# Kernel optimization log

Hardware: AMD Instinct MI355X
Metric: run time of the kernel (lower is better)

The kernel has to match this reference:

```python
import jax, jax.numpy as jnp
import numpy as np

N, E, G, H, D = 50000, 800000, 64, 2, 128  # nodes, edges, graphs, heads, out_channels
NEG_SLOPE_ATT = 0.2   # GATv2 default negative_slope
NEG_SLOPE_OUT = 0.01  # torch.nn.LeakyReLU default
BN_EPS = 1e-5


def setup_inputs() -> dict:
    key = jax.random.key(0)
    ks = jax.random.split(key, 12)
    x = jax.random.normal(ks[0], (N, 1), jnp.float32)
    edge_index = jax.random.randint(ks[1], (2, E), 0, N, dtype=jnp.int64)
    edge_attr = jax.random.normal(ks[2], (E,), jnp.float32)
    batch = jnp.sort(jax.random.randint(ks[3], (N,), 0, G, dtype=jnp.int64))
    # GATv2Conv params: lin_l/lin_r: Linear(1, H*D) with bias; lin_edge: Linear(1, H*D) no bias
    Wl = jax.random.normal(ks[4], (1, H * D), jnp.float32) * 0.5
    bl = jax.random.normal(ks[5], (H * D,), jnp.float32) * 0.1
    Wr = jax.random.normal(ks[6], (1, H * D), jnp.float32) * 0.5
    br = jax.random.normal(ks[7], (H * D,), jnp.float32) * 0.1
    We = jax.random.normal(ks[8], (1, H * D), jnp.float32) * 0.5
    att = jax.random.normal(ks[9], (H, D), jnp.float32) * 0.5
    bias = jax.random.normal(ks[10], (D,), jnp.float32) * 0.1
    gamma = jnp.ones((D,), jnp.float32)
    beta = jnp.zeros((D,), jnp.float32)
    return {"x": x, "edge_index": edge_index, "edge_attr": edge_attr, "batch": batch,
            "Wl": Wl, "bl": bl, "Wr": Wr, "br": br, "We": We, "att": att,
            "bias": bias, "gamma": gamma, "beta": beta}


def reference(x, edge_index, edge_attr, batch, Wl, bl, Wr, br, We, att, bias, gamma, beta):
    n = x.shape[0]
    src, dst = edge_index[0], edge_index[1]  # message flows src -> dst
    # node transforms: [N, H, D]
    xl = (x @ Wl + bl).reshape(n, H, D)  # lin_l (source side, also the message value)
    xr = (x @ Wr + br).reshape(n, H, D)  # lin_r (destination side)
    # edge feature embedding: [E, H, D]
    ee = (edge_attr[:, None] @ We).reshape(-1, H, D)
    # GATv2 scoring: leaky_relu(x_j + x_i + e), then dot with attention vector
    m = jax.nn.leaky_relu(xl[src] + xr[dst] + ee, NEG_SLOPE_ATT)  # [E, H, D]
    alpha = jnp.einsum('ehd,hd->eh', m, att)  # [E, H]
    # scatter-softmax over incoming edges per destination node
    amax = jax.ops.segment_max(alpha, dst, num_segments=n)  # [N, H]
    ea = jnp.exp(alpha - amax[dst])
    denom = jax.ops.segment_sum(ea, dst, num_segments=n)
    alpha = ea / (denom[dst] + 1e-16)
    # weighted scatter-add aggregation of x_j
    out = jax.ops.segment_sum(xl[src] * alpha[..., None], dst, num_segments=n)  # [N, H, D]
    out = out.mean(axis=1) + bias  # concat=False -> head average, then conv bias
    # BatchNorm1d in training mode (biased variance over nodes)
    mean = out.mean(axis=0)
    var = ((out - mean) ** 2).mean(axis=0)
    out = (out - mean) * jax.lax.rsqrt(var + BN_EPS) * gamma + beta
    out = jax.nn.leaky_relu(out, NEG_SLOPE_OUT)
    # graph-level scatter_add pooling
    return jax.ops.segment_sum(out, batch, num_segments=G)  # [G, D]
```

## Files before the change

### kernel.cpp

```cpp
#include <hip/hip_runtime.h>
#include <math.h>

#define NN 50000
#define NE 800000
#define NG 64

#define CB    2048
#define NBLK  391
#define NBUCK 196

static_assert(NBLK * CB >= NE, "chunk cover");
static_assert((NBUCK - 1) == (NN - 1) / 256, "bucket count");
static_assert(NE % 8 == 0, "edge unroll");

#define WS_C     0
#define WS_ACC   16
#define WS_BNSUM (WS_ACC + 4*NN)
#define WS_BNSQ  (WS_BNSUM + 128)
#define WS_MOM   WS_BNSUM
#define WS_EX    (WS_BNSQ + 128)
#define WS_TOT   (WS_EX + 272)
#define WS_CNT   (WS_TOT + 256)
#define WS_SORT  (WS_CNT + 256*NBLK)
#define WS_END   (WS_SORT + 4*NE)
#define WS_NEED_BYTES ((size_t)WS_END * 4 + 256)

static_assert(((WS_SORT * 4) % 16) == 0, "sort 16B alignment");

#define STEP(wl_, wr_, we_, bb_, at_, xs_, xd_, ae_, acc_)                 \
  { float tt = fmaf(we_, ae_, bb_); tt = fmaf(wr_, xd_, tt);               \
    tt = fmaf(wl_, xs_, tt); acc_ = fmaf(fabsf(tt), at_, acc_); }

#define SMEM_WEIGHTS_DECL                                                  \
  __shared__ __align__(16) float sWl[256], sWr[256], sWe[256], sB[256], sAt[256];

#define SMEM_WEIGHTS_LOAD                                                  \
  { int t_ = threadIdx.x;                                                  \
    sWl[t_] = Wl[t_]; sWr[t_] = Wr[t_]; sWe[t_] = We[t_];                  \
    sB[t_] = bl[t_] + br[t_]; sAt[t_] = att[t_]; }                         \
  __syncthreads();

#define SCORES(xs_, xd_, ae_, accA, accB, out0, out1)                      \
  { float lin0 = fmaf(c0.x, xs_, fmaf(c0.y, xd_, fmaf(c0.z, ae_, c0.w))); \
    out0 = fmaf(0.4f, accA, 0.6f * lin0);                                  \
    float lin1 = fmaf(c1.x, xs_, fmaf(c1.y, xd_, fmaf(c1.z, ae_, c1.w))); \
    out1 = fmaf(0.4f, accB, 0.6f * lin1); }

#define STEP4(c, q0, q1, q2, q3)                                           \
  STEP(wl.c, wr.c, we.c, bb.c, at.c, xs0, xd0, ae0, q0)                    \
  STEP(wl.c, wr.c, we.c, bb.c, at.c, xs1, xd1, ae1, q1)                    \
  STEP(wl.c, wr.c, we.c, bb.c, at.c, xs2, xd2, ae2, q2)                    \
  STEP(wl.c, wr.c, we.c, bb.c, at.c, xs3, xd3, ae3, q3)

#define SCORE_CORE                                                         \
  int4 s4 = *(const int4*)&ei[base];                                       \
  int4 dd4 = *(const int4*)&ei[NE + base];                                 \
  float4 ae4 = *(const float4*)&eattr[base];                               \
  float xs0 = x[s4.x], xs1 = x[s4.y], xs2 = x[s4.z], xs3 = x[s4.w];        \
  float xd0 = x[dd4.x], xd1 = x[dd4.y], xd2 = x[dd4.z], xd3 = x[dd4.w];    \
  float ae0 = ae4.x, ae1 = ae4.y, ae2 = ae4.z, ae3 = ae4.w;

#define SCORE_LOOPS                                                        \
  float a00 = 0.f, a01 = 0.f, a02 = 0.f, a03 = 0.f;                        \
  float a10 = 0.f, a11 = 0.f, a12 = 0.f, a13 = 0.f;                        \
  _Pragma("unroll 2")                                                      \
  for (int j = 0; j < 128; j += 4) {                                       \
    float4 wl = *(const float4*)&sWl[j];                                   \
    float4 wr = *(const float4*)&sWr[j];                                   \
    float4 we = *(const float4*)&sWe[j];                                   \
    float4 bb = *(const float4*)&sB[j];                                    \
    float4 at = *(const float4*)&sAt[j];                                   \
    STEP4(x, a00, a01, a02, a03)                                           \
    STEP4(y, a00, a01, a02, a03)                                           \
    STEP4(z, a00, a01, a02, a03)                                           \
    STEP4(w, a00, a01, a02, a03)                                           \
  }                                                                        \
  _Pragma("unroll 2")                                                      \
  for (int j = 128; j < 256; j += 4) {                                     \
    float4 wl = *(const float4*)&sWl[j];                                   \
    float4 wr = *(const float4*)&sWr[j];                                   \
    float4 we = *(const float4*)&sWe[j];                                   \
    float4 bb = *(const float4*)&sB[j];                                    \
    float4 at = *(const float4*)&sAt[j];                                   \
    STEP4(x, a10, a11, a12, a13)                                           \
    STEP4(y, a10, a11, a12, a13)                                           \
    STEP4(z, a10, a11, a12, a13)                                           \
    STEP4(w, a10, a11, a12, a13)                                           \
  }                                                                        \
  float4 c0 = *(const float4*)&ws[WS_C];                                   \
  float4 c1 = *(const float4*)&ws[WS_C + 4];

#define STEP8(c, Q)                                                        \
  STEP(wl.c, wr.c, we.c, bb.c, at.c, xs0, xd0, ae0, Q##0)                  \
  STEP(wl.c, wr.c, we.c, bb.c, at.c, xs1, xd1, ae1, Q##1)                  \
  STEP(wl.c, wr.c, we.c, bb.c, at.c, xs2, xd2, ae2, Q##2)                  \
  STEP(wl.c, wr.c, we.c, bb.c, at.c, xs3, xd3, ae3, Q##3)                  \
  STEP(wl.c, wr.c, we.c, bb.c, at.c, xs4, xd4, ae4, Q##4)                  \
  STEP(wl.c, wr.c, we.c, bb.c, at.c, xs5, xd5, ae5, Q##5)                  \
  STEP(wl.c, wr.c, we.c, bb.c, at.c, xs6, xd6, ae6, Q##6)                  \
  STEP(wl.c, wr.c, we.c, bb.c, at.c, xs7, xd7, ae7, Q##7)

extern "C" __global__ __launch_bounds__(256)
void k_hist(const int* __restrict__ ei,
            const float* __restrict__ att, const float* __restrict__ Wl,
            const float* __restrict__ Wr, const float* __restrict__ We,
            const float* __restrict__ bl, const float* __restrict__ br,
            float* __restrict__ ws, float* __restrict__ out)
{
  __shared__ unsigned cnt[256];
  cnt[threadIdx.x] = 0u;
  __syncthreads();
  int base = blockIdx.x * CB + (int)threadIdx.x * 8;
  if (base < NE) {
    int4 a = *(const int4*)&ei[NE + base];
    int4 b = *(const int4*)&ei[NE + base + 4];
    atomicAdd(&cnt[((unsigned)a.x) >> 8], 1u);
    atomicAdd(&cnt[((unsigned)a.y) >> 8], 1u);
    atomicAdd(&cnt[((unsigned)a.z) >> 8], 1u);
    atomicAdd(&cnt[((unsigned)a.w) >> 8], 1u);
    atomicAdd(&cnt[((unsigned)b.x) >> 8], 1u);
    atomicAdd(&cnt[((unsigned)b.y) >> 8], 1u);
    atomicAdd(&cnt[((unsigned)b.z) >> 8], 1u);
    atomicAdd(&cnt[((unsigned)b.w) >> 8], 1u);
  }
  __syncthreads();
  unsigned* counts = (unsigned*)(ws + WS_CNT);
  counts[(size_t)threadIdx.x * NBLK + blockIdx.x] = cnt[threadIdx.x];
  int gid = blockIdx.x * 256 + (int)threadIdx.x;
  if (gid < NG * 128) out[gid] = 0.f;
  if (gid < 14) ws[WS_MOM + gid] = 0.f;
  if (blockIdx.x == 0) {
    __shared__ float red[4][256];
    int t = threadIdx.x;
    float a = att[t];
    red[0][t] = a * Wl[t];
    red[1][t] = a * Wr[t];
    red[2][t] = a * We[t];
    red[3][t] = a * (bl[t] + br[t]);
    __syncthreads();
    if (t < 8) {
      int k = t >> 1, h = t & 1;
      float s = 0.f;
      for (int d = 0; d < 128; ++d) s += red[k][h * 128 + d];
      ws[WS_C + h * 4 + k] = s;
    }
  }
}

extern "C" __global__ __launch_bounds__(256)
void k_scan1(float* __restrict__ ws)
{
  int b = blockIdx.x;
  int t = threadIdx.x;
  unsigned* row = (unsigned*)(ws + WS_CNT) + (size_t)b * NBLK;
  __shared__ unsigned sc[256];
  unsigned carry = 0;
  for (int c = 0; c < NBLK; c += 256) {
    int k = c + t;
    unsigned v = (k < NBLK) ? row[k] : 0u;
    sc[t] = v;
    __syncthreads();
    for (int o = 1; o < 256; o <<= 1) {
      unsigned u = (t >= o) ? sc[t - o] : 0u;
      __syncthreads();
      sc[t] += u;
      __syncthreads();
    }
    unsigned incl = sc[t];
    if (k < NBLK) row[k] = carry + incl - v;
    unsigned total = sc[255];
    __syncthreads();
    carry += total;
  }
  if (t == 0) ((unsigned*)(ws + WS_TOT))[b] = carry;
}

extern "C" __global__ __launch_bounds__(256)
void k_scan2(float* __restrict__ ws)
{
  int b = threadIdx.x;
  unsigned v = ((const unsigned*)(ws + WS_TOT))[b];
  __shared__ unsigned sc[256];
  sc[b] = v;
  __syncthreads();
  for (int o = 1; o < 256; o <<= 1) {
    unsigned u = (b >= o) ? sc[b - o] : 0u;
    __syncthreads();
    sc[b] += u;
    __syncthreads();
  }
  unsigned* ex = (unsigned*)(ws + WS_EX);
  ex[b] = sc[b] - v;
  if (b == 255) ex[256] = sc[b];
}

extern "C" __global__ __launch_bounds__(256, 2)
void k_score(const int* __restrict__ ei, const float* __restrict__ x,
             const float* __restrict__ eattr,
             const float* __restrict__ Wl, const float* __restrict__ Wr,
             const float* __restrict__ We, const float* __restrict__ bl,
             const float* __restrict__ br, const float* __restrict__ att,
             float* __restrict__ ws)
{
  SMEM_WEIGHTS_DECL
  __shared__ unsigned soff[256];
  { int t_ = threadIdx.x;
    sWl[t_] = Wl[t_]; sWr[t_] = Wr[t_]; sWe[t_] = We[t_];
    sB[t_] = bl[t_] + br[t_]; sAt[t_] = att[t_];
    const unsigned* counts = (const unsigned*)(ws + WS_CNT);
    const unsigned* ex = (const unsigned*)(ws + WS_EX);
    soff[t_] = ex[t_] + counts[(size_t)t_ * NBLK + blockIdx.x];
  }
  __syncthreads();
  int base = blockIdx.x * CB + (int)threadIdx.x * 8;
  if (base >= NE) return;
  int4 sa = *(const int4*)&ei[base];
  int4 sb = *(const int4*)&ei[base + 4];
  int4 da = *(const int4*)&ei[NE + base];
  int4 db = *(const int4*)&ei[NE + base + 4];
  float4 aea = *(const float4*)&eattr[base];
  float4 aeb = *(const float4*)&eattr[base + 4];
  float ae0 = aea.x, ae1 = aea.y, ae2 = aea.z, ae3 = aea.w;
  float ae4 = aeb.x, ae5 = aeb.y, ae6 = aeb.z, ae7 = aeb.w;
  float xs0 = x[sa.x], xs1 = x[sa.y], xs2 = x[sa.z], xs3 = x[sa.w];
  float xs4 = x[sb.x], xs5 = x[sb.y], xs6 = x[sb.z], xs7 = x[sb.w];
  float xd0 = x[da.x], xd1 = x[da.y], xd2 = x[da.z], xd3 = x[da.w];
  float xd4 = x[db.x], xd5 = x[db.y], xd6 = x[db.z], xd7 = x[db.w];
  float q0 = 0.f, q1 = 0.f, q2 = 0.f, q3 = 0.f;
  float q4 = 0.f, q5 = 0.f, q6 = 0.f, q7 = 0.f;
  float r0 = 0.f, r1 = 0.f, r2 = 0.f, r3 = 0.f;
  float r4 = 0.f, r5 = 0.f, r6 = 0.f, r7 = 0.f;
#pragma unroll 2
  for (int j = 0; j < 128; j += 4) {
    float4 wl = *(const float4*)&sWl[j];
    float4 wr = *(const float4*)&sWr[j];
    float4 we = *(const float4*)&sWe[j];
    float4 bb = *(const float4*)&sB[j];
    float4 at = *(const float4*)&sAt[j];
    STEP8(x, q) STEP8(y, q) STEP8(z, q) STEP8(w, q)
  }
#pragma unroll 2
  for (int j = 128; j < 256; j += 4) {
    float4 wl = *(const float4*)&sWl[j];
    float4 wr = *(const float4*)&sWr[j];
    float4 we = *(const float4*)&sWe[j];
    float4 bb = *(const float4*)&sB[j];
    float4 at = *(const float4*)&sAt[j];
    STEP8(x, r) STEP8(y, r) STEP8(z, r) STEP8(w, r)
  }
  float4 c0 = *(const float4*)&ws[WS_C];
  float4 c1 = *(const float4*)&ws[WS_C + 4];
  float4* srt = (float4*)(ws + WS_SORT);
  float s0, s1;
#define EPI(i, dv)                                                         \
  { SCORES(xs##i, xd##i, ae##i, q##i, r##i, s0, s1)                        \
    unsigned d_ = (unsigned)(dv);                                          \
    unsigned p_ = atomicAdd(&soff[d_ >> 8], 1u);                           \
    srt[p_] = make_float4(__expf(s0), __expf(s1), xs##i, __uint_as_float(d_)); }
  EPI(0, da.x) EPI(1, da.y) EPI(2, da.z) EPI(3, da.w)
  EPI(4, db.x) EPI(5, db.y) EPI(6, db.z) EPI(7, db.w)
#undef EPI
}

extern "C" __global__ __launch_bounds__(256)
void k_gather(float* __restrict__ ws)
{
  int b = blockIdx.x;
  const int t = threadIdx.x;
  __shared__ float acc[1024];
  acc[t] = 0.f; acc[256 + t] = 0.f; acc[512 + t] = 0.f; acc[768 + t] = 0.f;
  __syncthreads();
  const unsigned* ex = (const unsigned*)(ws + WS_EX);
  int lo = (int)ex[b], hi = (int)ex[b + 1];
  const float4* srt = (const float4*)(ws + WS_SORT);
  for (int i = lo + t; i < hi; i += 256) {
    float4 r = srt[i];
    int l4 = (int)(__float_as_uint(r.w) & 255u) * 4;
    atomicAdd(&acc[l4 + 0], r.x);
    atomicAdd(&acc[l4 + 1], r.y);
    atomicAdd(&acc[l4 + 2], r.x * r.z);
    atomicAdd(&acc[l4 + 3], r.y * r.z);
  }
  __syncthreads();
  int n = (b << 8) + t;
  float f1 = 0.f, f2 = 0.f, f3 = 0.f, f4 = 0.f;
  if (n < NN) {
    float4 A = make_float4(acc[t * 4], acc[t * 4 + 1], acc[t * 4 + 2], acc[t * 4 + 3]);
    *(float4*)&ws[WS_ACC + 4 * n] = A;
    float r0 = 1.f / (A.x + 1e-16f);
    float r1 = 1.f / (A.y + 1e-16f);
    f1 = A.x * r0; f2 = A.z * r0; f3 = A.y * r1; f4 = A.w * r1;
  }
  float pm[14] = { f1, f2, f3, f4,
                   f1*f1, f1*f2, f1*f3, f1*f4,
                   f2*f2, f2*f3, f2*f4,
                   f3*f3, f3*f4, f4*f4 };
#pragma unroll
  for (int k = 0; k < 14; ++k) {
    float v = pm[k];
#pragma unroll
    for (int m = 32; m >= 1; m >>= 1) v += __shfl_xor(v, m);
    pm[k] = v;
  }
  __shared__ float smom[56];
  int wid = t >> 6, lane = t & 63;
  if (lane == 0) {
#pragma unroll
    for (int k = 0; k < 14; ++k) smom[wid * 14 + k] = pm[k];
  }
  __syncthreads();
  if (t < 14) {
    float s = smom[t] + smom[14 + t] + smom[28 + t] + smom[42 + t];
    atomicAdd(&ws[WS_MOM + t], s);
  }
}

extern "C" __global__ __launch_bounds__(256)
void k4m_pool(const int* __restrict__ batch,
              const float* __restrict__ Wl, const float* __restrict__ bl,
              const float* __restrict__ bias, const float* __restrict__ gamma,
              const float* __restrict__ beta,
              float* __restrict__ ws, float* __restrict__ out)
{
  const int CHUNK = (NN + (int)gridDim.x - 1) / (int)gridDim.x;
  int n0 = blockIdx.x * CHUNK;
  if (n0 >= NN) return;
  int n1 = n0 + CHUNK; if (n1 > NN) n1 = NN;
  int t = threadIdx.x;
  int d = t & 127;
  int row = t >> 7;
  float S1 = ws[WS_MOM + 0], S2 = ws[WS_MOM + 1];
  float S3 = ws[WS_MOM + 2], S4 = ws[WS_MOM + 3];
  float M11 = ws[WS_MOM + 4], M12 = ws[WS_MOM + 5], M13 = ws[WS_MOM + 6];
  float M14 = ws[WS_MOM + 7], M22 = ws[WS_MOM + 8], M23 = ws[WS_MOM + 9];
  float M24 = ws[WS_MOM + 10], M33 = ws[WS_MOM + 11], M34 = ws[WS_MOM + 12];
  float M44 = ws[WS_MOM + 13];
  float g1 = 0.5f * bl[d], g2 = 0.5f * Wl[d];
  float g3 = 0.5f * bl[128 + d], g4 = 0.5f * Wl[128 + d];
  float g5 = bias[d];
  const float invN = 1.f / (float)NN;
  float dotS = g1 * S1 + g2 * S2 + g3 * S3 + g4 * S4;
  float mean = (dotS + (float)NN * g5) * invN;
  float sumsq = g1*g1*M11 + g2*g2*M22 + g3*g3*M33 + g4*g4*M44
              + 2.f*(g1*g2*M12 + g1*g3*M13 + g1*g4*M14
                   + g2*g3*M23 + g2*g4*M24 + g3*g4*M34)
              + 2.f*g5*dotS + (float)NN*g5*g5;
  float var = fmaf(sumsq, invN, -mean * mean);
  float scale = gamma[d] * rsqrtf(var + 1e-5f);
  float shift = fmaf(-mean, scale, beta[d]);
  __shared__ float pool[4][128];
  for (int i = t; i < 512; i += 256) ((float*)pool)[i] = 0.f;
  __syncthreads();
  int g0 = batch[n0];
  for (int n = n0 + row; n < n1; n += 2) {
    float4 a = *(const float4*)&ws[WS_ACC + 4 * n];
    float r0 = 1.f / (a.x + 1e-16f);
    float r1 = 1.f / (a.y + 1e-16f);
    float o = g1 * (a.x * r0) + g2 * (a.z * r0)
            + g3 * (a.y * r1) + g4 * (a.w * r1) + g5;
    float v = fmaf(o, scale, shift);
    v = v > 0.f ? v : 0.01f * v;
    int g = batch[n];
    int slot = g - g0;
    if (slot < 4) atomicAdd(&pool[slot][d], v);
    else atomicAdd(&out[g * 128 + d], v);
  }
  __syncthreads();
  for (int i = t; i < 512; i += 256) {
    int slot = i >> 7, dd = i & 127;
    int g = g0 + slot;
    float v = pool[slot][dd];
    if (g < NG && v != 0.f) atomicAdd(&out[g * 128 + dd], v);
  }
}

extern "C" __global__ __launch_bounds__(256)
void k0_init(float* __restrict__ ws,
             const float* __restrict__ att, const float* __restrict__ Wl,
             const float* __restrict__ Wr, const float* __restrict__ We,
             const float* __restrict__ bl, const float* __restrict__ br,
             float* __restrict__ out)
{
  int tid = blockIdx.x * 256 + threadIdx.x;
  int nt = gridDim.x * 256;
  for (int i = tid; i < 4 * NN; i += nt) ws[WS_ACC + i] = 0.f;
  for (int i = tid; i < 256; i += nt) ws[WS_BNSUM + i] = 0.f;
  for (int i = tid; i < NG * 128; i += nt) out[i] = 0.f;
  if (blockIdx.x == 0) {
    __shared__ float red[4][256];
    int t = threadIdx.x;
    float a = att[t];
    red[0][t] = a * Wl[t];
    red[1][t] = a * Wr[t];
    red[2][t] = a * We[t];
    red[3][t] = a * (bl[t] + br[t]);
    __syncthreads();
    if (t < 8) {
      int k = t >> 1, h = t & 1;
      float s = 0.f;
      for (int d = 0; d < 128; ++d) s += red[k][h * 128 + d];
      ws[WS_C + h * 4 + k] = s;
    }
  }
}

extern "C" __global__ __launch_bounds__(256)
void k12f(const int* __restrict__ ei, const float* __restrict__ x,
          const float* __restrict__ eattr,
          const float* __restrict__ Wl, const float* __restrict__ Wr,
          const float* __restrict__ We, const float* __restrict__ bl,
          const float* __restrict__ br, const float* __restrict__ att,
          float* __restrict__ ws)
{
  SMEM_WEIGHTS_DECL
  SMEM_WEIGHTS_LOAD
  int base = (blockIdx.x * 256 + threadIdx.x) * 4;
  if (base >= NE) return;
  SCORE_CORE
  SCORE_LOOPS
  float* acc = ws + WS_ACC;
  float s0, s1;
#define EPI2(xs_, xd_, ae_, accA, accB, dsti)                              \
  { SCORES(xs_, xd_, ae_, accA, accB, s0, s1)                              \
    float e0 = __expf(s0), e1 = __expf(s1);                                \
    float* a = &acc[4 * dsti];                                             \
    atomicAdd(a + 0, e0); atomicAdd(a + 1, e1);                            \
    atomicAdd(a + 2, e0 * xs_); atomicAdd(a + 3, e1 * xs_); }
  EPI2(xs0, xd0, ae0, a00, a10, dd4.x)
  EPI2(xs1, xd1, ae1, a01, a11, dd4.y)
  EPI2(xs2, xd2, ae2, a02, a12, dd4.z)
  EPI2(xs3, xd3, ae3, a03, a13, dd4.w)
#undef EPI2
}

__device__ __forceinline__ float node_out4(float4 a, float wl0, float wl1,
                                           float b0, float b1, float bs)
{
  float r0 = 1.f / (a.x + 1e-16f);
  float r1 = 1.f / (a.y + 1e-16f);
  return 0.5f * (fmaf(wl0, a.z * r0, b0 * (a.x * r0)) +
                 fmaf(wl1, a.w * r1, b1 * (a.y * r1))) + bs;
}

extern "C" __global__ __launch_bounds__(256)
void k3_stats(const float* __restrict__ Wl, const float* __restrict__ bl,
              const float* __restrict__ bias, float* __restrict__ ws)
{
  int d = threadIdx.x & 127;
  int row = threadIdx.x >> 7;
  float wl0 = Wl[d], wl1 = Wl[128 + d];
  float b0 = bl[d], b1 = bl[128 + d];
  float bs = bias[d];
  float sum = 0.f, sq = 0.f;
  for (int n = blockIdx.x * 2 + row; n < NN; n += gridDim.x * 2) {
    float4 a = *(const float4*)&ws[WS_ACC + 4 * n];
    float o = node_out4(a, wl0, wl1, b0, b1, bs);
    sum += o;
    sq = fmaf(o, o, sq);
  }
  __shared__ float l1[256], l2[256];
  l1[threadIdx.x] = sum; l2[threadIdx.x] = sq;
  __syncthreads();
  if (row == 0) {
    atomicAdd(&ws[WS_BNSUM + d], l1[d] + l1[128 + d]);
    atomicAdd(&ws[WS_BNSQ + d], l2[d] + l2[128 + d]);
  }
}

extern "C" __global__ __launch_bounds__(256)
void k4_pool(const int* __restrict__ batch,
             const float* __restrict__ Wl, const float* __restrict__ bl,
             const float* __restrict__ bias, const float* __restrict__ gamma,
             const float* __restrict__ beta,
             float* __restrict__ ws, float* __restrict__ out)
{
  const int CHUNK = (NN + (int)gridDim.x - 1) / (int)gridDim.x;
  int n0 = blockIdx.x * CHUNK;
  if (n0 >= NN) return;
  int n1 = n0 + CHUNK; if (n1 > NN) n1 = NN;
  int d = threadIdx.x & 127;
  int row = threadIdx.x >> 7;
  const float invN = 1.f / (float)NN;
  float mean = ws[WS_BNSUM + d] * invN;
  float var = fmaf(ws[WS_BNSQ + d], invN, -mean * mean);
  float scale = gamma[d] * rsqrtf(var + 1e-5f);
  float shift = fmaf(-mean, scale, beta[d]);
  float wl0 = Wl[d], wl1 = Wl[128 + d];
  float b0 = bl[d], b1 = bl[128 + d];
  float bs = bias[d];
  __shared__ float pool[4][128];
  for (int i = threadIdx.x; i < 512; i += 256) ((float*)pool)[i] = 0.f;
  __syncthreads();
  int g0 = batch[n0];
  for (int n = n0 + row; n < n1; n += 2) {
    float4 a = *(const float4*)&ws[WS_ACC + 4 * n];
    float o = node_out4(a, wl0, wl1, b0, b1, bs);
    float v = fmaf(o, scale, shift);
    v = v > 0.f ? v : 0.01f * v;
    int g = batch[n];
    int slot = g - g0;
    if (slot < 4) atomicAdd(&pool[slot][d], v);
    else atomicAdd(&out[g * 128 + d], v);
  }
  __syncthreads();
  for (int i = threadIdx.x; i < 512; i += 256) {
    int slot = i >> 7, dd = i & 127;
    int g = g0 + slot;
    float v = pool[slot][dd];
    if (g < NG && v != 0.f) atomicAdd(&out[g * 128 + dd], v);
  }
}

extern "C" void kernel_launch(void* const* d_in, const int* in_sizes, int n_in,
                              void* d_out, int out_size, void* d_ws, size_t ws_size,
                              hipStream_t stream) {
  const float* x     = (const float*)d_in[0];
  const int*   ei    = (const int*)d_in[1];
  const float* eattr = (const float*)d_in[2];
  const int*   batch = (const int*)d_in[3];
  const float* Wl    = (const float*)d_in[4];
  const float* bl    = (const float*)d_in[5];
  const float* Wr    = (const float*)d_in[6];
  const float* br    = (const float*)d_in[7];
  const float* We    = (const float*)d_in[8];
  const float* att   = (const float*)d_in[9];
  const float* bias  = (const float*)d_in[10];
  const float* gam   = (const float*)d_in[11];
  const float* bet   = (const float*)d_in[12];
  float* ws  = (float*)d_ws;
  float* out = (float*)d_out;

  const bool dense = (ws_size >= WS_NEED_BYTES);

  if (dense) {
    hipLaunchKernelGGL(k_hist, dim3(NBLK), dim3(256), 0, stream,
                       ei, att, Wl, Wr, We, bl, br, ws, out);
    hipLaunchKernelGGL(k_scan1, dim3(256), dim3(256), 0, stream, ws);
    hipLaunchKernelGGL(k_scan2, dim3(1), dim3(256), 0, stream, ws);
    hipLaunchKernelGGL(k_score, dim3(NBLK), dim3(256), 0, stream,
                       ei, x, eattr, Wl, Wr, We, bl, br, att, ws);
    hipLaunchKernelGGL(k_gather, dim3(NBUCK), dim3(256), 0, stream, ws);
    hipLaunchKernelGGL(k4m_pool, dim3(256), dim3(256), 0, stream,
                       batch, Wl, bl, bias, gam, bet, ws, out);
  } else {
    hipLaunchKernelGGL(k0_init, dim3(128), dim3(256), 0, stream,
                       ws, att, Wl, Wr, We, bl, br, out);
    hipLaunchKernelGGL(k12f, dim3((NE / 4 + 255) / 256), dim3(256), 0, stream,
                       ei, x, eattr, Wl, Wr, We, bl, br, att, ws);
    hipLaunchKernelGGL(k3_stats, dim3(256), dim3(256), 0, stream,
                       Wl, bl, bias, ws);
    hipLaunchKernelGGL(k4_pool, dim3(256), dim3(256), 0, stream,
                       batch, Wl, bl, bias, gam, bet, ws, out);
  }
}
```

Measured before the change: 188.4 us.

## Halve edges per thread in scoring, read weights from global, precompute bias sum

```diff
diff --git a/kernel.cpp b/kernel.cpp
--- a/kernel.cpp
+++ b/kernel.cpp
@@ -5,13 +5,13 @@
 #define NE 800000
 #define NG 64
 
-#define CB    2048
-#define NBLK  391
+#define CB    1024
+#define NBLK  782
 #define NBUCK 196
 
 static_assert(NBLK * CB >= NE, "chunk cover");
 static_assert((NBUCK - 1) == (NN - 1) / 256, "bucket count");
-static_assert(NE % 8 == 0, "edge unroll");
+static_assert(NE % 4 == 0, "edge unroll");
 
 #define WS_C     0
 #define WS_ACC   16
@@ -20,7 +20,8 @@
 #define WS_MOM   WS_BNSUM
 #define WS_EX    (WS_BNSQ + 128)
 #define WS_TOT   (WS_EX + 272)
-#define WS_CNT   (WS_TOT + 256)
+#define WS_BSUM  (WS_TOT + 256)
+#define WS_CNT   (WS_BSUM + 256)
 #define WS_SORT  (WS_CNT + 256*NBLK)
 #define WS_END   (WS_SORT + 4*NE)
 #define WS_NEED_BYTES ((size_t)WS_END * 4 + 256)
@@ -90,16 +91,6 @@
   float4 c0 = *(const float4*)&ws[WS_C];                                   \
   float4 c1 = *(const float4*)&ws[WS_C + 4];
 
-#define STEP8(c, Q)                                                        \
-  STEP(wl.c, wr.c, we.c, bb.c, at.c, xs0, xd0, ae0, Q##0)                  \
-  STEP(wl.c, wr.c, we.c, bb.c, at.c, xs1, xd1, ae1, Q##1)                  \
-  STEP(wl.c, wr.c, we.c, bb.c, at.c, xs2, xd2, ae2, Q##2)                  \
-  STEP(wl.c, wr.c, we.c, bb.c, at.c, xs3, xd3, ae3, Q##3)                  \
-  STEP(wl.c, wr.c, we.c, bb.c, at.c, xs4, xd4, ae4, Q##4)                  \
-  STEP(wl.c, wr.c, we.c, bb.c, at.c, xs5, xd5, ae5, Q##5)                  \
-  STEP(wl.c, wr.c, we.c, bb.c, at.c, xs6, xd6, ae6, Q##6)                  \
-  STEP(wl.c, wr.c, we.c, bb.c, at.c, xs7, xd7, ae7, Q##7)
-
 extern "C" __global__ __launch_bounds__(256)
 void k_hist(const int* __restrict__ ei,
             const float* __restrict__ att, const float* __restrict__ Wl,
@@ -110,18 +101,13 @@
   __shared__ unsigned cnt[256];
   cnt[threadIdx.x] = 0u;
   __syncthreads();
-  int base = blockIdx.x * CB + (int)threadIdx.x * 8;
+  int base = blockIdx.x * CB + (int)threadIdx.x * 4;
   if (base < NE) {
     int4 a = *(const int4*)&ei[NE + base];
-    int4 b = *(const int4*)&ei[NE + base + 4];
     atomicAdd(&cnt[((unsigned)a.x) >> 8], 1u);
     atomicAdd(&cnt[((unsigned)a.y) >> 8], 1u);
     atomicAdd(&cnt[((unsigned)a.z) >> 8], 1u);
     atomicAdd(&cnt[((unsigned)a.w) >> 8], 1u);
-    atomicAdd(&cnt[((unsigned)b.x) >> 8], 1u);
-    atomicAdd(&cnt[((unsigned)b.y) >> 8], 1u);
-    atomicAdd(&cnt[((unsigned)b.z) >> 8], 1u);
-    atomicAdd(&cnt[((unsigned)b.w) >> 8], 1u);
   }
   __syncthreads();
   unsigned* counts = (unsigned*)(ws + WS_CNT);
@@ -130,8 +116,9 @@
   if (gid < NG * 128) out[gid] = 0.f;
   if (gid < 14) ws[WS_MOM + gid] = 0.f;
   if (blockIdx.x == 0) {
+    int t = threadIdx.x;
+    ws[WS_BSUM + t] = bl[t] + br[t];
     __shared__ float red[4][256];
-    int t = threadIdx.x;
     float a = att[t];
     red[0][t] = a * Wl[t];
     red[1][t] = a * Wr[t];
@@ -198,67 +185,57 @@
 void k_score(const int* __restrict__ ei, const float* __restrict__ x,
              const float* __restrict__ eattr,
              const float* __restrict__ Wl, const float* __restrict__ Wr,
-             const float* __restrict__ We, const float* __restrict__ bl,
-             const float* __restrict__ br, const float* __restrict__ att,
+             const float* __restrict__ We, const float* __restrict__ att,
+             const float* __restrict__ bsum,
              float* __restrict__ ws)
 {
-  SMEM_WEIGHTS_DECL
   __shared__ unsigned soff[256];
   { int t_ = threadIdx.x;
-    sWl[t_] = Wl[t_]; sWr[t_] = Wr[t_]; sWe[t_] = We[t_];
-    sB[t_] = bl[t_] + br[t_]; sAt[t_] = att[t_];
     const unsigned* counts = (const unsigned*)(ws + WS_CNT);
     const unsigned* ex = (const unsigned*)(ws + WS_EX);
     soff[t_] = ex[t_] + counts[(size_t)t_ * NBLK + blockIdx.x];
   }
   __syncthreads();
-  int base = blockIdx.x * CB + (int)threadIdx.x * 8;
+  int base = blockIdx.x * CB + (int)threadIdx.x * 4;
   if (base >= NE) return;
-  int4 sa = *(const int4*)&ei[base];
-  int4 sb = *(const int4*)&ei[base + 4];
-  int4 da = *(const int4*)&ei[NE + base];
-  int4 db = *(const int4*)&ei[NE + base + 4];
-  float4 aea = *(const float4*)&eattr[base];
-  float4 aeb = *(const float4*)&eattr[base + 4];
-  float ae0 = aea.x, ae1 = aea.y, ae2 = aea.z, ae3 = aea.w;
-  float ae4 = aeb.x, ae5 = aeb.y, ae6 = aeb.z, ae7 = aeb.w;
-  float xs0 = x[sa.x], xs1 = x[sa.y], xs2 = x[sa.z], xs3 = x[sa.w];
-  float xs4 = x[sb.x], xs5 = x[sb.y], xs6 = x[sb.z], xs7 = x[sb.w];
-  float xd0 = x[da.x], xd1 = x[da.y], xd2 = x[da.z], xd3 = x[da.w];
-  float xd4 = x[db.x], xd5 = x[db.y], xd6 = x[db.z], xd7 = x[db.w];
-  float q0 = 0.f, q1 = 0.f, q2 = 0.f, q3 = 0.f;
-  float q4 = 0.f, q5 = 0.f, q6 = 0.f, q7 = 0.f;
-  float r0 = 0.f, r1 = 0.f, r2 = 0.f, r3 = 0.f;
-  float r4 = 0.f, r5 = 0.f, r6 = 0.f, r7 = 0.f;
+  SCORE_CORE
+  float a00 = 0.f, a01 = 0.f, a02 = 0.f, a03 = 0.f;
+  float a10 = 0.f, a11 = 0.f, a12 = 0.f, a13 = 0.f;
 #pragma unroll 2
   for (int j = 0; j < 128; j += 4) {
-    float4 wl = *(const float4*)&sWl[j];
-    float4 wr = *(const float4*)&sWr[j];
-    float4 we = *(const float4*)&sWe[j];
-    float4 bb = *(const float4*)&sB[j];
-    float4 at = *(const float4*)&sAt[j];
-    STEP8(x, q) STEP8(y, q) STEP8(z, q) STEP8(w, q)
+    float4 wl = *(const float4*)&Wl[j];
+    float4 wr = *(const float4*)&Wr[j];
+    float4 we = *(const float4*)&We[j];
+    float4 bb = *(const float4*)&bsum[j];
+    float4 at = *(const float4*)&att[j];
+    STEP4(x, a00, a01, a02, a03)
+    STEP4(y, a00, a01, a02, a03)
+    STEP4(z, a00, a01, a02, a03)
+    STEP4(w, a00, a01, a02, a03)
   }
 #pragma unroll 2
   for (int j = 128; j < 256; j += 4) {
-    float4 wl = *(const float4*)&sWl[j];
-    float4 wr = *(const float4*)&sWr[j];
-    float4 we = *(const float4*)&sWe[j];
-    float4 bb = *(const float4*)&sB[j];
-    float4 at = *(const float4*)&sAt[j];
-    STEP8(x, r) STEP8(y, r) STEP8(z, r) STEP8(w, r)
+    float4 wl = *(const float4*)&Wl[j];
+    float4 wr = *(const float4*)&Wr[j];
+    float4 we = *(const float4*)&We[j];
+    float4 bb = *(const float4*)&bsum[j];
+    float4 at = *(const float4*)&att[j];
+    STEP4(x, a10, a11, a12, a13)
+    STEP4(y, a10, a11, a12, a13)
+    STEP4(z, a10, a11, a12, a13)
+    STEP4(w, a10, a11, a12, a13)
   }
   float4 c0 = *(const float4*)&ws[WS_C];
   float4 c1 = *(const float4*)&ws[WS_C + 4];
   float4* srt = (float4*)(ws + WS_SORT);
   float s0, s1;
-#define EPI(i, dv)                                                         \
-  { SCORES(xs##i, xd##i, ae##i, q##i, r##i, s0, s1)                        \
+#define EPI(i, dv, qa, qb)                                                 \
+  { SCORES(xs##i, xd##i, ae##i, qa, qb, s0, s1)                            \
     unsigned d_ = (unsigned)(dv);                                          \
     unsigned p_ = atomicAdd(&soff[d_ >> 8], 1u);                           \
     srt[p_] = make_float4(__expf(s0), __expf(s1), xs##i, __uint_as_float(d_)); }
-  EPI(0, da.x) EPI(1, da.y) EPI(2, da.z) EPI(3, da.w)
-  EPI(4, db.x) EPI(5, db.y) EPI(6, db.z) EPI(7, db.w)
+  EPI(0, dd4.x, a00, a10) EPI(1, dd4.y, a01, a11)
+  EPI(2, dd4.z, a02, a12) EPI(3, dd4.w, a03, a13)
 #undef EPI
 }
 
@@ -538,7 +515,8 @@
     hipLaunchKernelGGL(k_scan1, dim3(256), dim3(256), 0, stream, ws);
     hipLaunchKernelGGL(k_scan2, dim3(1), dim3(256), 0, stream, ws);
     hipLaunchKernelGGL(k_score, dim3(NBLK), dim3(256), 0, stream,
-                       ei, x, eattr, Wl, Wr, We, bl, br, att, ws);
+                       ei, x, eattr, Wl, Wr, We, att,
+                       (const float*)(ws + WS_BSUM), ws);
     hipLaunchKernelGGL(k_gather, dim3(NBUCK), dim3(256), 0, stream, ws);
     hipLaunchKernelGGL(k4m_pool, dim3(256), dim3(256), 0, stream,
                        batch, Wl, bl, bias, gam, bet, ws, out);
```

After: 189.6 us. No clear change (+0.6%).
